# Kernel optimization log

Measured on AMD Instinct MI355X. Metric: run time of the kernel, lower is better.

Reference implementation:

```python
import jax, jax.numpy as jnp
import numpy as np

D_MODEL = 1024
NUM_HEADS = 16
D_K = D_MODEL // NUM_HEADS


def setup_inputs() -> dict:
    key = jax.random.key(0)
    ks = jax.random.split(key, 13)
    B, S = 2, 2048
    s = 1.0 / np.sqrt(D_MODEL)
    inp = {
        'q': jax.random.normal(ks[0], (B, S, D_MODEL), jnp.float32),
        'k': jax.random.normal(ks[1], (B, S, D_MODEL), jnp.float32),
        'v': jax.random.normal(ks[2], (B, S, D_MODEL), jnp.float32),
        'mask': jax.random.randint(ks[3], (B, S), 0, 2, jnp.int32),
        'Wq': jax.random.normal(ks[4], (D_MODEL, D_MODEL), jnp.float32) * s,
        'bq': jax.random.normal(ks[5], (D_MODEL,), jnp.float32) * s,
        'Wk': jax.random.normal(ks[6], (D_MODEL, D_MODEL), jnp.float32) * s,
        'bk': jax.random.normal(ks[7], (D_MODEL,), jnp.float32) * s,
        'Wv': jax.random.normal(ks[8], (D_MODEL, D_MODEL), jnp.float32) * s,
        'bv': jax.random.normal(ks[9], (D_MODEL,), jnp.float32) * s,
        'Wo': jax.random.normal(ks[10], (D_MODEL, D_MODEL), jnp.float32) * s,
        'bo': jax.random.normal(ks[11], (D_MODEL,), jnp.float32) * s,
    }
    return inp


def reference(q, k, v, mask, Wq, bq, Wk, bk, Wv, bv, Wo, bo):
    B, S, _ = q.shape

    def split(x):  # [B,S,D] -> [B,H,S,d_k]
        return x.reshape(B, -1, NUM_HEADS, D_K).transpose(0, 2, 1, 3)

    qh = split(q @ Wq.T + bq)
    kh = split(k @ Wk.T + bk)
    vh = split(v @ Wv.T + bv)

    scores = jnp.einsum('bhqd,bhkd->bhqk', qh, kh) / jnp.sqrt(jnp.float32(D_K))
    scores = jnp.where(mask[:, None, None, :] == 0, jnp.float32(-1e9), scores)
    attn = jax.nn.softmax(scores, axis=-1)
    out = jnp.einsum('bhqk,bhkd->bhqd', attn, vh)  # [B,H,S,d_k]
    out = out.transpose(0, 2, 1, 3).reshape(B, S, NUM_HEADS * D_K)
    return out @ Wo.T + bo
```

## Files before the change

### kernel.cpp

```cpp
#include <hip/hip_runtime.h>
#include <cstdint>
#include <cstddef>


using bf16   = __bf16;
using bf16x4 = __attribute__((ext_vector_type(4))) __bf16;
using bf16x8 = __attribute__((ext_vector_type(8))) __bf16;
using f32x4  = __attribute__((ext_vector_type(4))) float;

#define MFMA_BF16(a, b, c) __builtin_amdgcn_mfma_f32_16x16x32_bf16((a), (b), (c), 0, 0, 0)

__device__ __forceinline__ void gload_lds16(const void* g, void* l) {
  __builtin_amdgcn_global_load_lds((__attribute__((address_space(1))) void*)g,
                                   (__attribute__((address_space(3))) void*)l,
                                   16, 0, 0);
}

#define CVT_PK(d, lo, hi) \
  asm("v_cvt_pk_bf16_f32 %0, %1, %2" : "=v"(d) : "v"(lo), "v"(hi))
#define SWAP32(x, y) \
  asm("v_permlane32_swap_b32 %0, %1" : "+v"(x), "+v"(y))
#define SWAP16(x, y) \
  asm("v_permlane16_swap_b32 %0, %1" : "+v"(x), "+v"(y))

#define LOG2E 1.4426950408889634f

__global__ __launch_bounds__(256) void prep_kernel(
    const float* __restrict__ q, const float* __restrict__ k, const float* __restrict__ v,
    const int* __restrict__ mask,
    const float* __restrict__ Wq, const float* __restrict__ Wk,
    const float* __restrict__ Wv, const float* __restrict__ Wo,
    bf16* __restrict__ qb, bf16* __restrict__ kb, bf16* __restrict__ vb,
    bf16* __restrict__ Wqb, bf16* __restrict__ Wkb, bf16* __restrict__ Wvb,
    bf16* __restrict__ Wob, float* __restrict__ maskf)
{
  const int NQ = 1048576;
  const int NW = 262144;
  const int STRIDE = 8194 * 256;
#pragma unroll
  for (int s = 0; s < 2; ++s) {
    int i = blockIdx.x * 256 + threadIdx.x + s * STRIDE;
    if (i < 3 * NQ) {
      const float* src; bf16* dst; int j;
      if (i < NQ)        { src = q; dst = qb; j = i; }
      else if (i < 2*NQ) { src = k; dst = kb; j = i - NQ; }
      else               { src = v; dst = vb; j = i - 2*NQ; }
      float4 f = ((const float4*)src)[j];
      ((bf16x4*)dst)[j] = bf16x4{(bf16)f.x, (bf16)f.y, (bf16)f.z, (bf16)f.w};
    } else if (i < 3*NQ + 4*NW) {
      int j = i - 3*NQ;
      const float* src; bf16* dst;
      if (j < NW)        { src = Wq; dst = Wqb; }
      else if (j < 2*NW) { src = Wk; dst = Wkb; j -= NW; }
      else if (j < 3*NW) { src = Wv; dst = Wvb; j -= 2*NW; }
      else               { src = Wo; dst = Wob; j -= 3*NW; }
      float4 f = ((const float4*)src)[j];
      ((bf16x4*)dst)[j] = bf16x4{(bf16)f.x, (bf16)f.y, (bf16)f.z, (bf16)f.w};
    } else if (i < 3*NQ + 4*NW + 1024) {
      int j = i - 3*NQ - 4*NW;
      int4 mi = ((const int4*)mask)[j];
      float4 o;
      o.x = (mi.x == 0) ? -1e9f * LOG2E : 0.0f;
      o.y = (mi.y == 0) ? -1e9f * LOG2E : 0.0f;
      o.z = (mi.z == 0) ? -1e9f * LOG2E : 0.0f;
      o.w = (mi.w == 0) ? -1e9f * LOG2E : 0.0f;
      ((float4*)maskf)[j] = o;
    }
  }
}

__global__ __launch_bounds__(256, 3) void proj3_kernel(
    const bf16* __restrict__ Xq, const bf16* __restrict__ Xk, const bf16* __restrict__ Xv,
    const bf16* __restrict__ Wqb, const bf16* __restrict__ Wkb, const bf16* __restrict__ Wvb,
    const float* __restrict__ bq, const float* __restrict__ bk, const float* __restrict__ bv,
    bf16* __restrict__ qh, bf16* __restrict__ kh, bf16* __restrict__ vhT)
{
  __shared__ bf16 As[128 * 64];
  __shared__ bf16 Bs[128 * 64];

  const int bid = blockIdx.x;
  const int z   = bid >> 8;
  const int r_  = bid & 255;

  const int tid = threadIdx.x, w = tid >> 6, lane = tid & 63;
  const int wr = w >> 1, wc = w & 1;
  const int quad = lane >> 4, l16 = lane & 15;
  const int sw = l16 & 7;
  const int srow8 = lane >> 3;
  const int scol  = ((lane & 7) ^ srow8) * 8;

  const bf16* Aptr; const bf16* Bptr;
  int m0, n0;
  if (z == 2) { Aptr = Wvb; Bptr = Xv; m0 = (r_ >> 5) * 128; n0 = (r_ & 31) * 128; }
  else        { Aptr = (z == 0) ? Xq : Xk; Bptr = (z == 0) ? Wqb : Wkb;
                m0 = (r_ >> 3) * 128; n0 = (r_ & 7) * 128; }

  f32x4 acc[4][4];
#pragma unroll
  for (int mt = 0; mt < 4; ++mt)
#pragma unroll
    for (int nt = 0; nt < 4; ++nt)
      acc[mt][nt] = f32x4{0.f, 0.f, 0.f, 0.f};

  for (int k0 = 0; k0 < 1024; k0 += 64) {
#pragma unroll
    for (int c8 = 0; c8 < 8; ++c8) {
      const int c = w * 8 + c8;
      if (c < 16) {
        const int row = c * 8 + srow8;
        gload_lds16(Aptr + (size_t)(m0 + row) * 1024 + k0 + scol, As + c * 512);
      } else {
        const int cB = c - 16;
        const int row = cB * 8 + srow8;
        gload_lds16(Bptr + (size_t)(n0 + row) * 1024 + k0 + scol, Bs + cB * 512);
      }
    }
    __syncthreads();
#pragma unroll
    for (int kk = 0; kk < 2; ++kk) {
      bf16x8 af[4], bf[4];
#pragma unroll
      for (int mt = 0; mt < 4; ++mt)
        af[mt] = *(const bf16x8*)(As + (wr*64 + mt*16 + l16) * 64 + ((kk*4 + quad) ^ sw) * 8);
#pragma unroll
      for (int nt = 0; nt < 4; ++nt)
        bf[nt] = *(const bf16x8*)(Bs + (wc*64 + nt*16 + l16) * 64 + ((kk*4 + quad) ^ sw) * 8);
#pragma unroll
      for (int mt = 0; mt < 4; ++mt)
#pragma unroll
        for (int nt = 0; nt < 4; ++nt)
          acc[mt][nt] = MFMA_BF16(af[mt], bf[nt], acc[mt][nt]);
    }
    __syncthreads();
  }

  if (z == 2) {
#pragma unroll
    for (int mt = 0; mt < 4; ++mt) {
      const int dvb = m0 + wr*64 + mt*16 + quad*4;
      const float4 bv4 = *(const float4*)(bv + dvb);
#pragma unroll
      for (int nt = 0; nt < 4; ++nt) {
        const int tok = n0 + wc*64 + nt*16 + l16;
        const int bb = tok >> 11, s = tok & 2047;
#pragma unroll
        for (int r = 0; r < 4; ++r) {
          const int dv = dvb + r;
          const int h = dv >> 6, d = dv & 63;
          vhT[(((size_t)bb*16 + h)*64 + d)*2048 + s] = (bf16)(acc[mt][nt][r] + (&bv4.x)[r]);
        }
      }
    }
  } else {
    const float* bias = (z == 0) ? bq : bk;
#pragma unroll
    for (int mt = 0; mt < 4; ++mt) {
#pragma unroll
      for (int nt = 0; nt < 4; ++nt) {
        const int n = n0 + wc*64 + nt*16 + l16;
        const int h = n >> 6, d = n & 63;
        const float bn = bias[n];
#pragma unroll
        for (int r = 0; r < 4; ++r) {
          const int m  = m0 + wr*64 + mt*16 + quad*4 + r;
          const int bb = m >> 11, s = m & 2047;
          const float val = acc[mt][nt][r] + bn;
          if (z == 0)
            qh[(((size_t)bb*16 + h)*2048 + s)*64 + d] = (bf16)(val * (0.125f * LOG2E));
          else
            kh[(((size_t)bb*16 + h)*2048 + s)*64 + d] = (bf16)val;
        }
      }
    }
  }
}


#define ATTN_BODY(T, FKC, FKN, MKC, MKN)                                        \
  {                                                                             \
    if ((T) < 30) stageTo((T) + 2, kvnn);                                       \
    if ((T) < 31) {                                                             \
      _Pragma("unroll")                                                         \
      for (int mb = 0; mb < 4; ++mb)                                            \
        MKN[mb] = *(const float4*)(mbase + ((T) + 1) * 64 + mb * 16);           \
      const char* pA = kvb + kvnxt + laneA;                                     \
      const char* pB = kvb + kvnxt + laneB;                                     \
      _Pragma("unroll")                                                         \
      for (int mb = 0; mb < 4; ++mb) {                                          \
        FKN[mb*2+0] = *(const bf16x8*)(pA + mb*2048);                           \
        FKN[mb*2+1] = *(const bf16x8*)(pB + mb*2048);                           \
      }                                                                         \
    }                                                                           \
    bf16x8 fV[8];                                                               \
    {                                                                           \
      const char* pA = kvb + kvcur + 8192 + laneA;                              \
      const char* pB = kvb + kvcur + 8192 + laneB;                              \
      _Pragma("unroll")                                                         \
      for (int mb = 0; mb < 4; ++mb) {                                          \
        fV[mb*2+0] = *(const bf16x8*)(pA + mb*2048);                            \
        fV[mb*2+1] = *(const bf16x8*)(pB + mb*2048);                            \
      }                                                                         \
    }                                                                           \
    _Pragma("unroll")                                                           \
    for (int rb = 0; rb < 2; ++rb) {                                            \
      f32x4 sac[4];                                                             \
      _Pragma("unroll")                                                         \
      for (int mb = 0; mb < 4; ++mb)                                            \
        sac[mb] = f32x4{MKC[mb].x, MKC[mb].y, MKC[mb].z, MKC[mb].w};            \
      _Pragma("unroll")                                                         \
      for (int kk = 0; kk < 2; ++kk)                                            \
        _Pragma("unroll")                                                       \
        for (int mb = 0; mb < 4; ++mb)                                          \
          sac[mb] = MFMA_BF16(FKC[mb*2+kk], aQ[rb][kk], sac[mb]);               \
      float p[4][4];                                                            \
      _Pragma("unroll")                                                         \
      for (int mb = 0; mb < 4; ++mb) {                                          \
        _Pragma("unroll")                                                       \
        for (int r = 0; r < 4; ++r) p[mb][r] = __builtin_amdgcn_exp2f(sac[mb][r]); \
        lacc[rb] += f32x4{p[mb][0], p[mb][1], p[mb][2], p[mb][3]};              \
      }                                                                         \
      uint32_t pk0[4], pk1[4];                                                  \
      _Pragma("unroll")                                                         \
      for (int mb = 0; mb < 4; ++mb) {                                          \
        CVT_PK(pk0[mb], p[mb][0], p[mb][1]);                                    \
        CVT_PK(pk1[mb], p[mb][2], p[mb][3]);                                    \
      }                                                                         \
      _Pragma("unroll")                                                         \
      for (int kk = 0; kk < 2; ++kk) {                                          \
        uint32_t a0 = pk0[2*kk], b0 = pk0[2*kk+1];                              \
        uint32_t a1 = pk1[2*kk], b1 = pk1[2*kk+1];                              \
        SWAP32(a0, b0); SWAP16(a0, b0);                                         \
        SWAP32(a1, b1); SWAP16(a1, b1);                                         \
        union { uint32_t u[4]; bf16x8 v; } un;                                  \
        un.u[0] = a0; un.u[1] = a1; un.u[2] = b0; un.u[3] = b1;                 \
        _Pragma("unroll")                                                       \
        for (int mb = 0; mb < 4; ++mb)                                          \
          Oacc[rb][mb] = MFMA_BF16(fV[mb*2+kk], un.v, Oacc[rb][mb]);            \
      }                                                                         \
    }                                                                           \
    __syncthreads();                                                            \
    { int tmp_ = kvcur; kvcur = kvnxt; kvnxt = kvnn; kvnn = tmp_; }             \
  }

__global__ __launch_bounds__(256, 2) void attn_kernel(
    const bf16* __restrict__ qh, const bf16* __restrict__ kh,
    const bf16* __restrict__ vhT, const float* __restrict__ maskf,
    bf16* __restrict__ out)
{
  __shared__ bf16 KV[3][2][4096];

  const int tid = threadIdx.x, w = tid >> 6, lane = tid & 63;
  const int quad = lane >> 4, l16 = lane & 15;
  const int sw = l16 & 7;
  const int srow8 = lane >> 3;
  const int scol  = ((lane & 7) ^ srow8) * 8;

  const int L  = blockIdx.x;
  const int bh = (L & 7) + ((L >> 7) << 3);
  const int qt = (L >> 3) & 15;
  const int b  = bh >> 4, h = bh & 15;
  const int q0 = qt * 128 + w * 32;

  const bf16* kbase = kh  + (size_t)bh * 2048 * 64;
  const bf16* vbase = vhT + (size_t)bh * 64 * 2048;
  const bf16* qbase = qh  + ((size_t)bh * 2048 + q0) * 64;
  const float* mbase = maskf + (size_t)b * 2048 + quad * 4;

  char* kvb = (char*)&KV[0][0][0];

  auto stageTo = [&](int t, int bufoff) {
    const int kt0 = t * 64;
#pragma unroll
    for (int c2 = 0; c2 < 2; ++c2) {
      const int c   = w * 2 + c2;
      const int row = c * 8 + srow8;
      gload_lds16(kbase + (size_t)(kt0 + row) * 64 + scol, kvb + bufoff + c * 1024);
      gload_lds16(vbase + (size_t)row * 2048 + kt0 + scol, kvb + bufoff + 8192 + c * 1024);
    }
  };

  bf16x8 aQ[2][2];
#pragma unroll
  for (int rb = 0; rb < 2; ++rb)
#pragma unroll
    for (int kk = 0; kk < 2; ++kk)
      aQ[rb][kk] = *(const bf16x8*)(qbase + (size_t)(rb*16 + l16)*64 + kk*32 + quad*8);

  const int laneA = l16 * 128 + ((quad    ) ^ sw) * 16;
  const int laneB = l16 * 128 + ((quad + 4) ^ sw) * 16;

  f32x4 Oacc[2][4];
  f32x4 lacc[2];
#pragma unroll
  for (int rb = 0; rb < 2; ++rb) {
    lacc[rb] = f32x4{0.f, 0.f, 0.f, 0.f};
#pragma unroll
    for (int mb = 0; mb < 4; ++mb) Oacc[rb][mb] = f32x4{0.f, 0.f, 0.f, 0.f};
  }

  stageTo(0, 0);
  stageTo(1, 16384);
  float4 mkA[4], mkB[4];
#pragma unroll
  for (int mb = 0; mb < 4; ++mb) mkA[mb] = *(const float4*)(mbase + mb*16);
  __syncthreads();

  bf16x8 fKa[8], fKb[8];
  {
    const char* pA = kvb + laneA;
    const char* pB = kvb + laneB;
#pragma unroll
    for (int mb = 0; mb < 4; ++mb) {
      fKa[mb*2+0] = *(const bf16x8*)(pA + mb*2048);
      fKa[mb*2+1] = *(const bf16x8*)(pB + mb*2048);
    }
  }

  int kvcur = 0, kvnxt = 16384, kvnn = 32768;

  for (int tt = 0; tt < 32; tt += 2) {
    ATTN_BODY(tt,     fKa, fKb, mkA, mkB);
    ATTN_BODY(tt + 1, fKb, fKa, mkB, mkA);
  }

#pragma unroll
  for (int rb = 0; rb < 2; ++rb) {
    float l_ = lacc[rb][0] + lacc[rb][1] + lacc[rb][2] + lacc[rb][3];
    l_ += __shfl_xor(l_, 16);
    l_ += __shfl_xor(l_, 32);
    const float inv = 1.0f / l_;
#pragma unroll
    for (int mb = 0; mb < 4; ++mb) {
      bf16x4 o = bf16x4{(bf16)(Oacc[rb][mb][0]*inv), (bf16)(Oacc[rb][mb][1]*inv),
                        (bf16)(Oacc[rb][mb][2]*inv), (bf16)(Oacc[rb][mb][3]*inv)};
      *(bf16x4*)(out + ((size_t)b*2048 + q0 + rb*16 + l16)*1024 + h*64 + mb*16 + quad*4) = o;
    }
  }
}

__global__ __launch_bounds__(256) void oproj_kernel(
    const bf16* __restrict__ Ain, const bf16* __restrict__ Wob,
    const float* __restrict__ bo, float* __restrict__ out)
{
  __shared__ bf16 As[64 * 64];
  __shared__ bf16 Bs[128 * 64];
  const int m0 = blockIdx.x * 64, n0 = blockIdx.y * 128;

  const int tid = threadIdx.x, w = tid >> 6, lane = tid & 63;
  const int quad = lane >> 4, l16 = lane & 15;
  const int sw = l16 & 7;
  const int srow8 = lane >> 3;
  const int scol  = ((lane & 7) ^ srow8) * 8;

  f32x4 acc[4][2];
#pragma unroll
  for (int mt = 0; mt < 4; ++mt)
#pragma unroll
    for (int nt = 0; nt < 2; ++nt)
      acc[mt][nt] = f32x4{0.f, 0.f, 0.f, 0.f};

  for (int k0 = 0; k0 < 1024; k0 += 64) {
#pragma unroll
    for (int c4 = 0; c4 < 6; ++c4) {
      const int c = w * 6 + c4;
      if (c < 8) {
        const int row = c * 8 + srow8;
        gload_lds16(Ain + (size_t)(m0 + row) * 1024 + k0 + scol, As + c * 512);
      } else {
        const int cB = c - 8;
        const int row = cB * 8 + srow8;
        gload_lds16(Wob + (size_t)(n0 + row) * 1024 + k0 + scol, Bs + cB * 512);
      }
    }
    __syncthreads();
#pragma unroll
    for (int kk = 0; kk < 2; ++kk) {
      bf16x8 af[4], bfr[2];
#pragma unroll
      for (int mt = 0; mt < 4; ++mt)
        af[mt] = *(const bf16x8*)(As + (mt*16 + l16) * 64 + ((kk*4 + quad) ^ sw) * 8);
#pragma unroll
      for (int nt = 0; nt < 2; ++nt)
        bfr[nt] = *(const bf16x8*)(Bs + (w*32 + nt*16 + l16) * 64 + ((kk*4 + quad) ^ sw) * 8);
#pragma unroll
      for (int mt = 0; mt < 4; ++mt)
#pragma unroll
        for (int nt = 0; nt < 2; ++nt)
          acc[mt][nt] = MFMA_BF16(af[mt], bfr[nt], acc[mt][nt]);
    }
    __syncthreads();
  }

#pragma unroll
  for (int mt = 0; mt < 4; ++mt) {
#pragma unroll
    for (int nt = 0; nt < 2; ++nt) {
      const int n = n0 + w*32 + nt*16 + l16;
      const float bn = bo[n];
#pragma unroll
      for (int r = 0; r < 4; ++r) {
        const int m = m0 + mt*16 + quad*4 + r;
        out[(size_t)m * 1024 + n] = acc[mt][nt][r] + bn;
      }
    }
  }
}

extern "C" void kernel_launch(void* const* d_in, const int* in_sizes, int n_in,
                              void* d_out, int out_size, void* d_ws, size_t ws_size,
                              hipStream_t stream)
{
  const float* q    = (const float*)d_in[0];
  const float* k    = (const float*)d_in[1];
  const float* v    = (const float*)d_in[2];
  const int*   mask = (const int*)d_in[3];
  const float* Wq   = (const float*)d_in[4];
  const float* bq   = (const float*)d_in[5];
  const float* Wk   = (const float*)d_in[6];
  const float* bk   = (const float*)d_in[7];
  const float* Wv   = (const float*)d_in[8];
  const float* bv   = (const float*)d_in[9];
  const float* Wo   = (const float*)d_in[10];
  const float* bo   = (const float*)d_in[11];

  char* ws = (char*)d_ws;
  bf16*  qb    = (bf16*)(ws);
  bf16*  kb    = (bf16*)(ws + (8ull  << 20));
  bf16*  vb    = (bf16*)(ws + (16ull << 20));
  bf16*  Wqb   = (bf16*)(ws + (24ull << 20));
  bf16*  Wkb   = (bf16*)(ws + (26ull << 20));
  bf16*  Wvb   = (bf16*)(ws + (28ull << 20));
  bf16*  Wob   = (bf16*)(ws + (30ull << 20));
  float* maskf = (float*)(ws + (32ull << 20));
  bf16*  qh    = (bf16*)(ws + (33ull << 20));
  bf16*  kh    = (bf16*)(ws + (41ull << 20));
  bf16*  vhT   = (bf16*)(ws + (49ull << 20));
  bf16*  ao    = (bf16*)(ws);
  float* out   = (float*)d_out;

  prep_kernel<<<8194, 256, 0, stream>>>(q, k, v, mask, Wq, Wk, Wv, Wo,
                                        qb, kb, vb, Wqb, Wkb, Wvb, Wob, maskf);
  proj3_kernel<<<768, 256, 0, stream>>>(qb, kb, vb, Wqb, Wkb, Wvb,
                                        bq, bk, bv, qh, kh, vhT);
  attn_kernel<<<512, 256, 0, stream>>>(qh, kh, vhT, maskf, ao);
  oproj_kernel<<<dim3(64, 8), 256, 0, stream>>>(ao, Wob, bo, out);
}
```

Measured before the change: 213.7 us.

## Compact unmasked keys via prefix scan and skip masked KV tiles in attention

Adds a scan kernel that computes per-batch prefix indices of unmasked keys, then projection writes K and V only for kept tokens into compacted positions. Attention iterates only over the tiles covering the kept count, skipping work for masked keys, with zero-padded tails and a compacted additive mask. The P-to-MFMA operand shuffle is also changed from permlane swaps to a round-trip through LDS. The compaction is valid whenever any key is unmasked and does not depend on the particular test inputs. It adds a small serial scan kernel and LDS traffic in the inner loop.

```diff
diff --git a/kernel.cpp b/kernel.cpp
--- a/kernel.cpp
+++ b/kernel.cpp
@@ -16,27 +16,78 @@
                                    16, 0, 0);
 }
 
-#define CVT_PK(d, lo, hi) \
-  asm("v_cvt_pk_bf16_f32 %0, %1, %2" : "=v"(d) : "v"(lo), "v"(hi))
-#define SWAP32(x, y) \
-  asm("v_permlane32_swap_b32 %0, %1" : "+v"(x), "+v"(y))
-#define SWAP16(x, y) \
-  asm("v_permlane16_swap_b32 %0, %1" : "+v"(x), "+v"(y))
-
 #define LOG2E 1.4426950408889634f
+
+__global__ __launch_bounds__(256) void scan_kernel(
+    const int* __restrict__ mask,
+    int* __restrict__ pref,
+    int* __restrict__ cnt,
+    float* __restrict__ maskc,
+    bf16* __restrict__ kh,
+    bf16* __restrict__ vhT)
+{
+  const int b = blockIdx.x;
+  const int tid = threadIdx.x;
+  __shared__ int sums[256];
+
+  const int base = b * 2048 + tid * 8;
+  int v[8]; int s_ = 0;
+#pragma unroll
+  for (int j = 0; j < 8; ++j) { v[j] = (mask[base + j] != 0) ? 1 : 0; s_ += v[j]; }
+  sums[tid] = s_;
+  __syncthreads();
+  for (int off = 1; off < 256; off <<= 1) {
+    int x = sums[tid];
+    int y = (tid >= off) ? sums[tid - off] : 0;
+    __syncthreads();
+    sums[tid] = x + y;
+    __syncthreads();
+  }
+  const int excl  = tid ? sums[tid - 1] : 0;
+  const int total = sums[255];
+  int run = excl;
+#pragma unroll
+  for (int j = 0; j < 8; ++j) { pref[base + j] = v[j] ? run : -1; run += v[j]; }
+  if (tid == 0) cnt[b] = total;
+
+  int nt2 = ((total + 127) >> 7) * 2;
+  if (nt2 < 2) nt2 = 2;
+  const int span = nt2 * 64;
+
+  for (int sc = tid; sc < 2048; sc += 256)
+    maskc[b * 2048 + sc] = (sc < total) ? 0.0f : -1e9f * LOG2E;
+
+  for (int idx = tid; idx < 16 * 128; idx += 256) {
+    const int h = idx >> 7, ro = idx & 127;
+    const int s = total + ro;
+    if (s < span) {
+      bf16* p = kh + (((size_t)(b * 16 + h) * 2048 + s) * 64);
+#pragma unroll
+      for (int d = 0; d < 64; d += 8)
+        *(bf16x8*)(p + d) = bf16x8{(bf16)0.f,(bf16)0.f,(bf16)0.f,(bf16)0.f,
+                                   (bf16)0.f,(bf16)0.f,(bf16)0.f,(bf16)0.f};
+    }
+  }
+  for (int j = tid; j < 16 * 64 * 128; j += 256) {
+    const int h = j >> 13, rem = j & 8191;
+    const int d = rem >> 7, co = rem & 127;
+    const int c = total + co;
+    if (c < span)
+      vhT[(((size_t)(b * 16 + h) * 64 + d) * 2048) + c] = (bf16)0.f;
+  }
+}
 
 __global__ __launch_bounds__(256) void prep_kernel(
     const float* __restrict__ q, const float* __restrict__ k, const float* __restrict__ v,
-    const int* __restrict__ mask,
     const float* __restrict__ Wq, const float* __restrict__ Wk,
     const float* __restrict__ Wv, const float* __restrict__ Wo,
     bf16* __restrict__ qb, bf16* __restrict__ kb, bf16* __restrict__ vb,
     bf16* __restrict__ Wqb, bf16* __restrict__ Wkb, bf16* __restrict__ Wvb,
-    bf16* __restrict__ Wob, float* __restrict__ maskf)
+    bf16* __restrict__ Wob)
 {
   const int NQ = 1048576;
   const int NW = 262144;
-  const int STRIDE = 8194 * 256;
+  const int STRIDE = 8192 * 256;
 #pragma unroll
   for (int s = 0; s < 2; ++s) {
     int i = blockIdx.x * 256 + threadIdx.x + s * STRIDE;
@@ -47,7 +98,7 @@
       else               { src = v; dst = vb; j = i - 2*NQ; }
       float4 f = ((const float4*)src)[j];
       ((bf16x4*)dst)[j] = bf16x4{(bf16)f.x, (bf16)f.y, (bf16)f.z, (bf16)f.w};
-    } else if (i < 3*NQ + 4*NW) {
+    } else {
       int j = i - 3*NQ;
       const float* src; bf16* dst;
       if (j < NW)        { src = Wq; dst = Wqb; }
@@ -56,15 +107,6 @@
       else               { src = Wo; dst = Wob; j -= 3*NW; }
       float4 f = ((const float4*)src)[j];
       ((bf16x4*)dst)[j] = bf16x4{(bf16)f.x, (bf16)f.y, (bf16)f.z, (bf16)f.w};
-    } else if (i < 3*NQ + 4*NW + 1024) {
-      int j = i - 3*NQ - 4*NW;
-      int4 mi = ((const int4*)mask)[j];
-      float4 o;
-      o.x = (mi.x == 0) ? -1e9f * LOG2E : 0.0f;
-      o.y = (mi.y == 0) ? -1e9f * LOG2E : 0.0f;
-      o.z = (mi.z == 0) ? -1e9f * LOG2E : 0.0f;
-      o.w = (mi.w == 0) ? -1e9f * LOG2E : 0.0f;
-      ((float4*)maskf)[j] = o;
     }
   }
 }
@@ -73,6 +115,7 @@
     const bf16* __restrict__ Xq, const bf16* __restrict__ Xk, const bf16* __restrict__ Xv,
     const bf16* __restrict__ Wqb, const bf16* __restrict__ Wkb, const bf16* __restrict__ Wvb,
     const float* __restrict__ bq, const float* __restrict__ bk, const float* __restrict__ bv,
+    const int* __restrict__ pref,
     bf16* __restrict__ qh, bf16* __restrict__ kh, bf16* __restrict__ vhT)
 {
   __shared__ bf16 As[128 * 64];
@@ -135,6 +178,10 @@
   }
 
   if (z == 2) {
+    int sc4[4];
+#pragma unroll
+    for (int nt = 0; nt < 4; ++nt)
+      sc4[nt] = pref[n0 + wc*64 + nt*16 + l16];
 #pragma unroll
     for (int mt = 0; mt < 4; ++mt) {
       const int dvb = m0 + wr*64 + mt*16 + quad*4;
@@ -142,44 +189,66 @@
 #pragma unroll
       for (int nt = 0; nt < 4; ++nt) {
         const int tok = n0 + wc*64 + nt*16 + l16;
-        const int bb = tok >> 11, s = tok & 2047;
-#pragma unroll
-        for (int r = 0; r < 4; ++r) {
-          const int dv = dvb + r;
-          const int h = dv >> 6, d = dv & 63;
-          vhT[(((size_t)bb*16 + h)*64 + d)*2048 + s] = (bf16)(acc[mt][nt][r] + (&bv4.x)[r]);
+        const int bb = tok >> 11;
+        if (sc4[nt] >= 0) {
+#pragma unroll
+          for (int r = 0; r < 4; ++r) {
+            const int dv = dvb + r;
+            const int h = dv >> 6, d = dv & 63;
+            vhT[(((size_t)bb*16 + h)*64 + d)*2048 + sc4[nt]] = (bf16)(acc[mt][nt][r] + (&bv4.x)[r]);
+          }
         }
       }
     }
-  } else {
-    const float* bias = (z == 0) ? bq : bk;
+  } else if (z == 0) {
 #pragma unroll
     for (int mt = 0; mt < 4; ++mt) {
 #pragma unroll
       for (int nt = 0; nt < 4; ++nt) {
         const int n = n0 + wc*64 + nt*16 + l16;
         const int h = n >> 6, d = n & 63;
-        const float bn = bias[n];
+        const float bn = bq[n];
 #pragma unroll
         for (int r = 0; r < 4; ++r) {
           const int m  = m0 + wr*64 + mt*16 + quad*4 + r;
           const int bb = m >> 11, s = m & 2047;
           const float val = acc[mt][nt][r] + bn;
-          if (z == 0)
-            qh[(((size_t)bb*16 + h)*2048 + s)*64 + d] = (bf16)(val * (0.125f * LOG2E));
-          else
-            kh[(((size_t)bb*16 + h)*2048 + s)*64 + d] = (bf16)val;
+          qh[(((size_t)bb*16 + h)*2048 + s)*64 + d] = (bf16)(val * (0.125f * LOG2E));
         }
       }
     }
-  }
-}
-
+  } else {
+#pragma unroll
+    for (int mt = 0; mt < 4; ++mt) {
+      int dst4[4];
+#pragma unroll
+      for (int r = 0; r < 4; ++r)
+        dst4[r] = pref[m0 + wr*64 + mt*16 + quad*4 + r];
+#pragma unroll
+      for (int nt = 0; nt < 4; ++nt) {
+        const int n = n0 + wc*64 + nt*16 + l16;
+        const int h = n >> 6, d = n & 63;
+        const float bn = bk[n];
+#pragma unroll
+        for (int r = 0; r < 4; ++r) {
+          const int m  = m0 + wr*64 + mt*16 + quad*4 + r;
+          const int bb = m >> 11;
+          if (dst4[r] >= 0) {
+            const float val = acc[mt][nt][r] + bn;
+            kh[(((size_t)bb*16 + h)*2048 + dst4[r])*64 + d] = (bf16)val;
+          }
+        }
+      }
+    }
+  }
+}
+
+#define PSTRIDE 72
 
 #define ATTN_BODY(T, FKC, FKN, MKC, MKN)                                        \
   {                                                                             \
-    if ((T) < 30) stageTo((T) + 2, kvnn);                                       \
-    if ((T) < 31) {                                                             \
+    if ((T) + 2 < nt2) stageTo((T) + 2, kvnn);                                  \
+    if ((T) + 1 < nt2) {                                                        \
       _Pragma("unroll")                                                         \
       for (int mb = 0; mb < 4; ++mb)                                            \
         MKN[mb] = *(const float4*)(mbase + ((T) + 1) * 64 + mb * 16);           \
@@ -219,23 +288,18 @@
         for (int r = 0; r < 4; ++r) p[mb][r] = __builtin_amdgcn_exp2f(sac[mb][r]); \
         lacc[rb] += f32x4{p[mb][0], p[mb][1], p[mb][2], p[mb][3]};              \
       }                                                                         \
-      uint32_t pk0[4], pk1[4];                                                  \
       _Pragma("unroll")                                                         \
       for (int mb = 0; mb < 4; ++mb) {                                          \
-        CVT_PK(pk0[mb], p[mb][0], p[mb][1]);                                    \
-        CVT_PK(pk1[mb], p[mb][2], p[mb][3]);                                    \
+        bf16x4 pk = bf16x4{(bf16)p[mb][0], (bf16)p[mb][1],                      \
+                           (bf16)p[mb][2], (bf16)p[mb][3]};                     \
+        *(bf16x4*)(bW + mb*16) = pk;                                            \
       }                                                                         \
       _Pragma("unroll")                                                         \
       for (int kk = 0; kk < 2; ++kk) {                                          \
-        uint32_t a0 = pk0[2*kk], b0 = pk0[2*kk+1];                              \
-        uint32_t a1 = pk1[2*kk], b1 = pk1[2*kk+1];                              \
-        SWAP32(a0, b0); SWAP16(a0, b0);                                         \
-        SWAP32(a1, b1); SWAP16(a1, b1);                                         \
-        union { uint32_t u[4]; bf16x8 v; } un;                                  \
-        un.u[0] = a0; un.u[1] = a1; un.u[2] = b0; un.u[3] = b1;                 \
+        bf16x8 aP = *(const bf16x8*)(bR + kk*32);                               \
         _Pragma("unroll")                                                       \
         for (int mb = 0; mb < 4; ++mb)                                          \
-          Oacc[rb][mb] = MFMA_BF16(fV[mb*2+kk], un.v, Oacc[rb][mb]);            \
+          Oacc[rb][mb] = MFMA_BF16(fV[mb*2+kk], aP, Oacc[rb][mb]);              \
       }                                                                         \
     }                                                                           \
     __syncthreads();                                                            \
@@ -244,10 +308,11 @@
 
 __global__ __launch_bounds__(256, 2) void attn_kernel(
     const bf16* __restrict__ qh, const bf16* __restrict__ kh,
-    const bf16* __restrict__ vhT, const float* __restrict__ maskf,
-    bf16* __restrict__ out)
+    const bf16* __restrict__ vhT, const float* __restrict__ maskc,
+    const int* __restrict__ cnt, bf16* __restrict__ out)
 {
   __shared__ bf16 KV[3][2][4096];
+  __shared__ bf16 Ps[4][16 * PSTRIDE];
 
   const int tid = threadIdx.x, w = tid >> 6, lane = tid & 63;
   const int quad = lane >> 4, l16 = lane & 15;
@@ -264,9 +329,14 @@
   const bf16* kbase = kh  + (size_t)bh * 2048 * 64;
   const bf16* vbase = vhT + (size_t)bh * 64 * 2048;
   const bf16* qbase = qh  + ((size_t)bh * 2048 + q0) * 64;
-  const float* mbase = maskf + (size_t)b * 2048 + quad * 4;
+  const float* mbase = maskc + (size_t)b * 2048 + quad * 4;
+
+  const int total = cnt[b];
+  int nt2 = ((total + 127) >> 7) * 2;
+  if (nt2 < 2) nt2 = 2;
 
   char* kvb = (char*)&KV[0][0][0];
+  bf16* Pw = Ps[w];
 
   auto stageTo = [&](int t, int bufoff) {
     const int kt0 = t * 64;
@@ -288,6 +358,8 @@
 
   const int laneA = l16 * 128 + ((quad    ) ^ sw) * 16;
   const int laneB = l16 * 128 + ((quad + 4) ^ sw) * 16;
+  bf16*       bW = Pw + l16 * PSTRIDE + quad * 4;
+  const bf16* bR = Pw + l16 * PSTRIDE + quad * 8;
 
   f32x4 Oacc[2][4];
   f32x4 lacc[2];
@@ -318,7 +390,7 @@
 
   int kvcur = 0, kvnxt = 16384, kvnn = 32768;
 
-  for (int tt = 0; tt < 32; tt += 2) {
+  for (int tt = 0; tt < nt2; tt += 2) {
     ATTN_BODY(tt,     fKa, fKb, mkA, mkB);
     ATTN_BODY(tt + 1, fKb, fKa, mkB, mkA);
   }
@@ -431,17 +503,20 @@
   bf16*  Wkb   = (bf16*)(ws + (26ull << 20));
   bf16*  Wvb   = (bf16*)(ws + (28ull << 20));
   bf16*  Wob   = (bf16*)(ws + (30ull << 20));
-  float* maskf = (float*)(ws + (32ull << 20));
+  float* maskc = (float*)(ws + (32ull << 20));
+  int*   pref  = (int*)(ws + (32ull << 20) + (64ull << 10));
+  int*   cnt   = (int*)(ws + (32ull << 20) + (128ull << 10));
   bf16*  qh    = (bf16*)(ws + (33ull << 20));
   bf16*  kh    = (bf16*)(ws + (41ull << 20));
   bf16*  vhT   = (bf16*)(ws + (49ull << 20));
   bf16*  ao    = (bf16*)(ws);
   float* out   = (float*)d_out;
 
-  prep_kernel<<<8194, 256, 0, stream>>>(q, k, v, mask, Wq, Wk, Wv, Wo,
-                                        qb, kb, vb, Wqb, Wkb, Wvb, Wob, maskf);
+  scan_kernel<<<2, 256, 0, stream>>>(mask, pref, cnt, maskc, kh, vhT);
+  prep_kernel<<<8192, 256, 0, stream>>>(q, k, v, Wq, Wk, Wv, Wo,
+                                        qb, kb, vb, Wqb, Wkb, Wvb, Wob);
   proj3_kernel<<<768, 256, 0, stream>>>(qb, kb, vb, Wqb, Wkb, Wvb,
-                                        bq, bk, bv, qh, kh, vhT);
-  attn_kernel<<<512, 256, 0, stream>>>(qh, kh, vhT, maskf, ao);
+                                        bq, bk, bv, pref, qh, kh, vhT);
+  attn_kernel<<<512, 256, 0, stream>>>(qh, kh, vhT, maskc, cnt, ao);
   oproj_kernel<<<dim3(64, 8), 256, 0, stream>>>(ao, Wob, bo, out);
 }
```

Result: slower. 228.3 us (+6.8%).
